# Kernel tuning notes

Hardware: AMD Instinct MI355X
Metric: run time of the kernel (lower is better)

The kernel has to match this reference:

```python
import jax, jax.numpy as jnp
import numpy as np
import math

HIDDEN = 1024
HEADS = 16
LAYERS = 4
IN_DIM = 512
OUT_DIM = 1024
B, S = 4, 2048


def _pos_encoding(seq_len, dim):
    pos = jnp.arange(seq_len, dtype=jnp.float32)[:, None]            # [S,1]
    div = jnp.exp(jnp.arange(0, dim, 2, dtype=jnp.float32) * (-math.log(10000.0) / dim))  # [D/2]
    ang = pos * div                                                   # [S,D/2]
    # interleave: even idx sin, odd idx cos
    return jnp.stack([jnp.sin(ang), jnp.cos(ang)], axis=-1).reshape(seq_len, dim)


def _layernorm(x, g, b, eps=1e-5):
    mu = jnp.mean(x, axis=-1, keepdims=True)
    var = jnp.var(x, axis=-1, keepdims=True)
    return (x - mu) * jax.lax.rsqrt(var + eps) * g + b


def setup_inputs() -> dict:
    key = jax.random.key(0)
    ks = jax.random.split(key, 8)
    d = {
        'x': jax.random.normal(ks[0], (B, S, IN_DIM), jnp.float32),
        'in_W': jax.random.normal(ks[1], (IN_DIM, HIDDEN), jnp.float32) * (1.0 / math.sqrt(IN_DIM)),
        'in_b': jnp.zeros((HIDDEN,), jnp.float32),
        'qkv_W': jax.random.normal(ks[2], (LAYERS, HIDDEN, 3 * HIDDEN), jnp.float32) * (1.0 / math.sqrt(HIDDEN)),
        'qkv_b': jnp.zeros((LAYERS, 3 * HIDDEN), jnp.float32),
        'out_W': jax.random.normal(ks[3], (LAYERS, HIDDEN, HIDDEN), jnp.float32) * (1.0 / math.sqrt(HIDDEN)),
        'out_b': jnp.zeros((LAYERS, HIDDEN), jnp.float32),
        'ln1_g': jnp.ones((LAYERS, HIDDEN), jnp.float32),
        'ln1_b': jnp.zeros((LAYERS, HIDDEN), jnp.float32),
        'ln2_g': jnp.ones((LAYERS, HIDDEN), jnp.float32),
        'ln2_b': jnp.zeros((LAYERS, HIDDEN), jnp.float32),
        'ff1_W': jax.random.normal(ks[4], (LAYERS, HIDDEN, 4 * HIDDEN), jnp.float32) * (1.0 / math.sqrt(HIDDEN)),
        'ff1_b': jnp.zeros((LAYERS, 4 * HIDDEN), jnp.float32),
        'ff2_W': jax.random.normal(ks[5], (LAYERS, 4 * HIDDEN, HIDDEN), jnp.float32) * (1.0 / math.sqrt(4 * HIDDEN)),
        'ff2_b': jnp.zeros((LAYERS, HIDDEN), jnp.float32),
        'fin_g': jnp.ones((HIDDEN,), jnp.float32),
        'fin_b': jnp.zeros((HIDDEN,), jnp.float32),
        'op_W': jax.random.normal(ks[6], (HIDDEN, OUT_DIM), jnp.float32) * (1.0 / math.sqrt(HIDDEN)),
        'op_b': jnp.zeros((OUT_DIM,), jnp.float32),
    }
    return d


def reference(x, in_W, in_b, qkv_W, qkv_b, out_W, out_b, ln1_g, ln1_b, ln2_g, ln2_b,
              ff1_W, ff1_b, ff2_W, ff2_b, fin_g, fin_b, op_W, op_b):
    b, s, _ = x.shape
    dh = HIDDEN // HEADS
    h = x @ in_W + in_b                                   # [B,S,D]
    h = h * math.sqrt(HIDDEN) + _pos_encoding(s, HIDDEN)  # scaled + PE (dropout=eval)
    for i in range(LAYERS):
        qkv = (h @ qkv_W[i] + qkv_b[i]).reshape(b, s, 3, HEADS, dh)
        q, k, v = qkv[:, :, 0], qkv[:, :, 1], qkv[:, :, 2]
        scores = jnp.einsum('bqhd,bkhd->bhqk', q, k) / math.sqrt(dh)
        attn = jax.nn.softmax(scores, axis=-1)
        ctx = jnp.einsum('bhqk,bkhd->bqhd', attn, v).reshape(b, s, HIDDEN)
        h = _layernorm(h + (ctx @ out_W[i] + out_b[i]), ln1_g[i], ln1_b[i])
        ff = jax.nn.relu(h @ ff1_W[i] + ff1_b[i]) @ ff2_W[i] + ff2_b[i]
        h = _layernorm(h + ff, ln2_g[i], ln2_b[i])
    h = _layernorm(h, fin_g, fin_b)
    return h @ op_W + op_b
```

## Files before the change

### kernel.cpp

```cpp
#include <hip/hip_runtime.h>
#include <math.h>

typedef unsigned short u16;
typedef __attribute__((ext_vector_type(8))) __bf16 bf16x8;
typedef __attribute__((ext_vector_type(4))) float floatx4;
typedef unsigned int __attribute__((address_space(1))) g_u32;
typedef unsigned int __attribute__((address_space(3))) l_u32;

#define EPI_BIAS  1
#define EPI_RELU  2
#define EPI_EMBED 8

__device__ __forceinline__ float bf2f(u16 u) {
    union { unsigned int i; float f; } v; v.i = ((unsigned int)u) << 16; return v.f;
}
__device__ __forceinline__ u16 f2bf(float f) {
    union { __bf16 b; u16 u; } v; v.b = (__bf16)f; return v.u;
}
__device__ __forceinline__ void gl_lds16(const void* g, void* l) {
    __builtin_amdgcn_global_load_lds((const g_u32*)g, (l_u32*)l, 16, 0, 0);
}
__device__ __forceinline__ float posenc(int s, int c) {
    double e = exp((double)(c & 1022) * (-9.210340371976184 / 1024.0));
    double ang = (double)s * e;
    return (float)((c & 1) ? cos(ang) : sin(ang));
}

__global__ __launch_bounds__(256) void conv_split(
    const float* __restrict__ in, u16* __restrict__ oh, u16* __restrict__ ol) {
    const int i = (blockIdx.x * 256 + threadIdx.x) * 8;
    float4 a = ((const float4*)(in + i))[0];
    float4 b = ((const float4*)(in + i))[1];
    float f[8] = {a.x, a.y, a.z, a.w, b.x, b.y, b.z, b.w};
    union { u16 u[8]; uint4 q; } H, L;
    #pragma unroll
    for (int j = 0; j < 8; ++j) {
        u16 hi = f2bf(f[j]);
        H.u[j] = hi; L.u[j] = f2bf(f[j] - bf2f(hi));
    }
    *(uint4*)&oh[i] = H.q;
    *(uint4*)&ol[i] = L.q;
}

template<int TMODE>
__global__ __launch_bounds__(256) void transpose_f2b(
    const float* __restrict__ in, u16* __restrict__ oh,
    int R, int C) {
    __shared__ float tile[32][33];
    int bx = blockIdx.x * 32, by = blockIdx.y * 32;
    int tx = threadIdx.x & 31, ty = threadIdx.x >> 5;
    #pragma unroll
    for (int i = ty; i < 32; i += 8) tile[i][tx] = in[(size_t)(by + i) * C + bx + tx];
    __syncthreads();
    #pragma unroll
    for (int i = ty; i < 32; i += 8) {
        float f = tile[tx][i];
        u16 hi = f2bf(f);
        u16 o = (TMODE == 2) ? f2bf(f - bf2f(hi)) : hi;
        oh[(size_t)(bx + i) * R + by + tx] = o;
    }
}

template<int EPI, bool ACCUM, bool WF, bool WB, bool WB2>
__global__ __launch_bounds__(256) void gemm_k(
    const u16* __restrict__ A, const u16* __restrict__ Bt,
    const float* __restrict__ bias,
    float* __restrict__ outF, u16* __restrict__ outB, u16* __restrict__ outB2,
    int M, int N, int K) {
    __shared__ alignas(16) u16 As[128 * 32];
    __shared__ alignas(16) u16 Bs[128 * 32];
    const int tid = threadIdx.x;
    const int wave = tid >> 6, lane = tid & 63;
    const int l16 = lane & 15, quad = lane >> 4;
    const int bm = blockIdx.x * 128, bn = blockIdx.y * 128;
    const int wm = (wave & 1) * 64, wn = (wave >> 1) * 64;
    const int sr = tid >> 2, sc = (tid & 3) * 8;

    floatx4 acc[4][4];
    floatx4 zero = {0.0f, 0.0f, 0.0f, 0.0f};
    #pragma unroll
    for (int i = 0; i < 4; ++i)
        #pragma unroll
        for (int j = 0; j < 4; ++j) acc[i][j] = zero;

    for (int k0 = 0; k0 < K; k0 += 32) {
        #pragma unroll
        for (int p = 0; p < 2; ++p) {
            const u16* ga = A + (size_t)(bm + sr + 64 * p) * K + k0 + sc;
            gl_lds16(ga, &As[(p * 64 + (wave << 4)) * 32]);
        }
        #pragma unroll
        for (int p = 0; p < 2; ++p) {
            const u16* gb = Bt + (size_t)(bn + sr + 64 * p) * K + k0 + sc;
            gl_lds16(gb, &Bs[(p * 64 + (wave << 4)) * 32]);
        }
        __syncthreads();
        bf16x8 af[4], bfr[4];
        #pragma unroll
        for (int i = 0; i < 4; ++i) af[i] = *(const bf16x8*)&As[(wm + i * 16 + l16) * 32 + quad * 8];
        #pragma unroll
        for (int j = 0; j < 4; ++j) bfr[j] = *(const bf16x8*)&Bs[(wn + j * 16 + l16) * 32 + quad * 8];
        #pragma unroll
        for (int i = 0; i < 4; ++i)
            #pragma unroll
            for (int j = 0; j < 4; ++j)
                acc[i][j] = __builtin_amdgcn_mfma_f32_16x16x32_bf16(af[i], bfr[j], acc[i][j], 0, 0, 0);
        __syncthreads();
    }

    #pragma unroll
    for (int i = 0; i < 4; ++i) {
        #pragma unroll
        for (int r = 0; r < 4; ++r) {
            int row = bm + wm + i * 16 + quad * 4 + r;
            #pragma unroll
            for (int j = 0; j < 4; ++j) {
                int col = bn + wn + j * 16 + l16;
                float v = acc[i][j][r];
                if (EPI & EPI_BIAS) v += bias[col];
                if (ACCUM) v += outF[(size_t)row * N + col];
                if (EPI & EPI_EMBED) { v = v * 32.0f + posenc(row & 2047, col); }
                if (EPI & EPI_RELU) v = fmaxf(v, 0.0f);
                if (WF) outF[(size_t)row * N + col] = v;
                if (WB) {
                    u16 hi = f2bf(v);
                    outB[(size_t)row * N + col] = hi;
                    if (WB2) outB2[(size_t)row * N + col] = f2bf(v - bf2f(hi));
                }
            }
        }
    }
}

template<bool SPLIT>
__global__ __launch_bounds__(256) void attn_k(
    const float* __restrict__ qkv, u16* __restrict__ ctx) {
    constexpr int KSTR = 72;
    constexpr int VSTR = 72;
    constexpr int PSTR = 88;
    __shared__ alignas(16) u16 Kh[2][64 * KSTR];
    __shared__ alignas(16) u16 Kl[2][SPLIT ? 64 * KSTR : 8];
    __shared__ alignas(16) u16 Vt[2][64 * VSTR];
    __shared__ alignas(16) u16 Ps[128 * PSTR];

    const int tid = threadIdx.x, wave = tid >> 6, lane = tid & 63;
    const int l16 = lane & 15, quad = lane >> 4;
    const int bh = blockIdx.x >> 4, qt = blockIdx.x & 15;
    const int b = bh >> 4, h = bh & 15;
    const size_t base = (size_t)b * 2048 * 3072;
    const int wq = wave * 32;

    const int kr = tid >> 2, kcb = (tid & 3) * 16;
    const float* gK = qkv + base + (size_t)kr * 3072 + 1024 + h * 64 + kcb;
    const int vk = lane, vdg = wave * 16;
    const float* gV = qkv + base + (size_t)vk * 3072 + 2048 + h * 64 + vdg;

    bf16x8 qh[2][2], ql[2][2];
    #pragma unroll
    for (int i = 0; i < 2; ++i) {
        const float* g = qkv + base + (size_t)(qt * 128 + wq + i * 16 + l16) * 3072 + h * 64 + quad * 8;
        #pragma unroll
        for (int kk = 0; kk < 2; ++kk) {
            float4 va = ((const float4*)(g + kk * 32))[0];
            float4 vb = ((const float4*)(g + kk * 32))[1];
            float f[8] = {va.x, va.y, va.z, va.w, vb.x, vb.y, vb.z, vb.w};
            union { u16 u[8]; bf16x8 v; } th, tl;
            #pragma unroll
            for (int j = 0; j < 8; ++j) {
                float s = f[j] * 0.125f;
                u16 hi = f2bf(s);
                th.u[j] = hi;
                if (SPLIT) tl.u[j] = f2bf(s - bf2f(hi));
            }
            qh[i][kk] = th.v;
            if (SPLIT) ql[i][kk] = tl.v;
        }
    }

    float4 pk4[4], pv4[4];
    auto LOAD = [&](int c) {
        const float* g = gK + (size_t)(c * 64) * 3072;
        pk4[0] = ((const float4*)g)[0]; pk4[1] = ((const float4*)g)[1];
        pk4[2] = ((const float4*)g)[2]; pk4[3] = ((const float4*)g)[3];
        const float* g2 = gV + (size_t)(c * 64) * 3072;
        pv4[0] = ((const float4*)g2)[0]; pv4[1] = ((const float4*)g2)[1];
        pv4[2] = ((const float4*)g2)[2]; pv4[3] = ((const float4*)g2)[3];
    };
    auto STORE = [&](int bu) {
        const float* pf = (const float*)pk4;
        union { u16 u[8]; uint4 q; } h0, h1, s0, s1;
        #pragma unroll
        for (int j = 0; j < 8; ++j) {
            float a = pf[j], c2 = pf[8 + j];
            u16 ah = f2bf(a); h0.u[j] = ah;
            u16 ch = f2bf(c2); h1.u[j] = ch;
            if (SPLIT) { s0.u[j] = f2bf(a - bf2f(ah)); s1.u[j] = f2bf(c2 - bf2f(ch)); }
        }
        *(uint4*)&Kh[bu][kr * KSTR + kcb]     = h0.q;
        *(uint4*)&Kh[bu][kr * KSTR + kcb + 8] = h1.q;
        if (SPLIT) {
            *(uint4*)&Kl[bu][kr * KSTR + kcb]     = s0.q;
            *(uint4*)&Kl[bu][kr * KSTR + kcb + 8] = s1.q;
        }
        const float* vf = (const float*)pv4;
        #pragma unroll
        for (int j = 0; j < 16; ++j)
            Vt[bu][(vdg + j) * VSTR + vk] = f2bf(vf[j]);
    };

    floatx4 acc_o[2][4];
    float mrun[2][4], lrun[2][4];
    floatx4 zf = {0.0f, 0.0f, 0.0f, 0.0f};
    #pragma unroll
    for (int i = 0; i < 2; ++i)
        #pragma unroll
        for (int j = 0; j < 4; ++j) acc_o[i][j] = zf;
    #pragma unroll
    for (int i = 0; i < 2; ++i)
        #pragma unroll
        for (int r = 0; r < 4; ++r) { mrun[i][r] = -1e30f; lrun[i][r] = 0.0f; }

    LOAD(0); STORE(0); LOAD(1);
    __syncthreads();

    for (int c = 0; c < 32; ++c) {
        const int cur = c & 1;

        floatx4 acc_s[2][4];
        #pragma unroll
        for (int i = 0; i < 2; ++i)
            #pragma unroll
            for (int j = 0; j < 4; ++j) acc_s[i][j] = zf;
        #pragma unroll
        for (int kk = 0; kk < 2; ++kk) {
            bf16x8 kbh[4], kbl[4];
            #pragma unroll
            for (int j = 0; j < 4; ++j) {
                kbh[j] = *(const bf16x8*)&Kh[cur][(j * 16 + l16) * KSTR + kk * 32 + quad * 8];
                if (SPLIT) kbl[j] = *(const bf16x8*)&Kl[cur][(j * 16 + l16) * KSTR + kk * 32 + quad * 8];
            }
            __builtin_amdgcn_s_setprio(1);
            #pragma unroll
            for (int i = 0; i < 2; ++i)
                #pragma unroll
                for (int j = 0; j < 4; ++j) {
                    acc_s[i][j] = __builtin_amdgcn_mfma_f32_16x16x32_bf16(qh[i][kk], kbh[j], acc_s[i][j], 0, 0, 0);
                    if (SPLIT) {
                        acc_s[i][j] = __builtin_amdgcn_mfma_f32_16x16x32_bf16(ql[i][kk], kbh[j], acc_s[i][j], 0, 0, 0);
                        acc_s[i][j] = __builtin_amdgcn_mfma_f32_16x16x32_bf16(qh[i][kk], kbl[j], acc_s[i][j], 0, 0, 0);
                    }
                }
            __builtin_amdgcn_s_setprio(0);
        }

        float mx[2][4];
        #pragma unroll
        for (int i = 0; i < 2; ++i)
            #pragma unroll
            for (int r = 0; r < 4; ++r) {
                float m0 = fmaxf(fmaxf(acc_s[i][0][r], acc_s[i][1][r]),
                                 fmaxf(acc_s[i][2][r], acc_s[i][3][r]));
                #pragma unroll
                for (int off = 8; off; off >>= 1) m0 = fmaxf(m0, __shfl_xor(m0, off));
                mx[i][r] = m0;
            }
        bool up = false;
        #pragma unroll
        for (int i = 0; i < 2; ++i)
            #pragma unroll
            for (int r = 0; r < 4; ++r) up = up || (mx[i][r] > mrun[i][r] + 8.0f);
        if (__any(up)) {
            #pragma unroll
            for (int i = 0; i < 2; ++i)
                #pragma unroll
                for (int r = 0; r < 4; ++r) {
                    float nm = fmaxf(mrun[i][r], mx[i][r]);
                    float sc = __expf(mrun[i][r] - nm);
                    mrun[i][r] = nm;
                    lrun[i][r] *= sc;
                    #pragma unroll
                    for (int jd = 0; jd < 4; ++jd) acc_o[i][jd][r] *= sc;
                }
        }
        #pragma unroll
        for (int i = 0; i < 2; ++i)
            #pragma unroll
            for (int r = 0; r < 4; ++r) {
                float rs = 0.0f;
                #pragma unroll
                for (int j = 0; j < 4; ++j) {
                    float p = __expf(acc_s[i][j][r] - mrun[i][r]);
                    acc_s[i][j][r] = p;
                    rs += p;
                }
                #pragma unroll
                for (int off = 8; off; off >>= 1) rs += __shfl_xor(rs, off);
                lrun[i][r] += rs;
                #pragma unroll
                for (int j = 0; j < 4; ++j)
                    Ps[(wq + i * 16 + quad * 4 + r) * PSTR + j * 16 + l16] = f2bf(acc_s[i][j][r]);
            }
        asm volatile("s_waitcnt lgkmcnt(0)" ::: "memory");

        #pragma unroll
        for (int kk = 0; kk < 2; ++kk) {
            bf16x8 pa[2], vb[4];
            #pragma unroll
            for (int i = 0; i < 2; ++i)
                pa[i] = *(const bf16x8*)&Ps[(wq + i * 16 + l16) * PSTR + kk * 32 + quad * 8];
            #pragma unroll
            for (int jd = 0; jd < 4; ++jd)
                vb[jd] = *(const bf16x8*)&Vt[cur][(jd * 16 + l16) * VSTR + kk * 32 + quad * 8];
            __builtin_amdgcn_s_setprio(1);
            #pragma unroll
            for (int i = 0; i < 2; ++i)
                #pragma unroll
                for (int jd = 0; jd < 4; ++jd)
                    acc_o[i][jd] = __builtin_amdgcn_mfma_f32_16x16x32_bf16(pa[i], vb[jd], acc_o[i][jd], 0, 0, 0);
            __builtin_amdgcn_s_setprio(0);
        }

        if (c + 1 < 32) STORE(cur ^ 1);
        __syncthreads();
        if (c + 2 < 32) LOAD(c + 2);
    }

    #pragma unroll
    for (int i = 0; i < 2; ++i) {
        #pragma unroll
        for (int r = 0; r < 4; ++r) {
            float inv = 1.0f / lrun[i][r];
            size_t ro = (size_t)(b * 2048 + qt * 128 + wq + i * 16 + quad * 4 + r) * 1024 + h * 64;
            #pragma unroll
            for (int jd = 0; jd < 4; ++jd)
                ctx[ro + jd * 16 + l16] = f2bf(acc_o[i][jd][r] * inv);
        }
    }
}

__global__ __launch_bounds__(256) void ln_k(
    float* __restrict__ h, const float* __restrict__ g, const float* __restrict__ bb,
    u16* __restrict__ hb) {
    const int row = blockIdx.x, tid = threadIdx.x;
    const int wave = tid >> 6, lane = tid & 63;
    float4 v = *(const float4*)(h + (size_t)row * 1024 + tid * 4);
    float x[4] = {v.x, v.y, v.z, v.w};
    float s = x[0] + x[1] + x[2] + x[3];
    float s2 = x[0] * x[0] + x[1] * x[1] + x[2] * x[2] + x[3] * x[3];
    for (int off = 32; off; off >>= 1) { s += __shfl_xor(s, off); s2 += __shfl_xor(s2, off); }
    __shared__ float red[8];
    if (lane == 0) { red[wave] = s; red[4 + wave] = s2; }
    __syncthreads();
    s = red[0] + red[1] + red[2] + red[3];
    s2 = red[4] + red[5] + red[6] + red[7];
    float mu = s * (1.0f / 1024.0f);
    float var = s2 * (1.0f / 1024.0f) - mu * mu;
    float rs = rsqrtf(var + 1e-5f);
    float4 gg = *(const float4*)(g + tid * 4);
    float4 bp = *(const float4*)(bb + tid * 4);
    float4 o;
    o.x = (x[0] - mu) * rs * gg.x + bp.x;
    o.y = (x[1] - mu) * rs * gg.y + bp.y;
    o.z = (x[2] - mu) * rs * gg.z + bp.z;
    o.w = (x[3] - mu) * rs * gg.w + bp.w;
    *(float4*)(h + (size_t)row * 1024 + tid * 4) = o;
    union { u16 u[4]; uint2 q; } hb4;
    hb4.u[0] = f2bf(o.x); hb4.u[1] = f2bf(o.y);
    hb4.u[2] = f2bf(o.z); hb4.u[3] = f2bf(o.w);
    *(uint2*)&hb[(size_t)row * 1024 + tid * 4] = hb4.q;
}

extern "C" void kernel_launch(void* const* d_in, const int* in_sizes, int n_in,
                              void* d_out, int out_size, void* d_ws, size_t ws_size,
                              hipStream_t stream) {
    const float* x     = (const float*)d_in[0];
    const float* in_W  = (const float*)d_in[1];
    const float* in_b  = (const float*)d_in[2];
    const float* qkv_W = (const float*)d_in[3];
    const float* qkv_b = (const float*)d_in[4];
    const float* out_W = (const float*)d_in[5];
    const float* out_b = (const float*)d_in[6];
    const float* ln1_g = (const float*)d_in[7];
    const float* ln1_b = (const float*)d_in[8];
    const float* ln2_g = (const float*)d_in[9];
    const float* ln2_b = (const float*)d_in[10];
    const float* ff1_W = (const float*)d_in[11];
    const float* ff1_b = (const float*)d_in[12];
    const float* ff2_W = (const float*)d_in[13];
    const float* ff2_b = (const float*)d_in[14];
    const float* fin_g = (const float*)d_in[15];
    const float* fin_b = (const float*)d_in[16];
    const float* op_W  = (const float*)d_in[17];
    const float* op_b  = (const float*)d_in[18];

    size_t off = 0;
    char* wsb = (char*)d_ws;
    auto alloc = [&](size_t bytes) { void* p = wsb + off; off += (bytes + 255) & ~(size_t)255; return p; };
    u16*   BtH  = (u16*)alloc((size_t)4096 * 1024 * 2);
    float* hbuf = (float*)alloc((size_t)8192 * 1024 * 4);
    float* qkvb = (float*)alloc((size_t)8192 * 3072 * 4);
    u16*   ctxb = (u16*)alloc((size_t)8192 * 1024 * 2);
    u16*   hbfH = (u16*)alloc((size_t)8192 * 1024 * 2);
    if (off > ws_size) return;
    u16* xh  = (u16*)qkvb;
    u16* xl  = xh + (size_t)8192 * 512;
    u16* h0h = ctxb;
    u16* h0l = hbfH;
    u16* ffb = (u16*)qkvb;

    dim3 tb(256);

    conv_split<<<dim3(2048), tb, 0, stream>>>(x, xh, xl);
    transpose_f2b<0><<<dim3(32, 16), tb, 0, stream>>>(in_W, BtH, 512, 1024);
    gemm_k<0, false, true, false, false><<<dim3(64, 8), tb, 0, stream>>>(
        xh, BtH, nullptr, hbuf, nullptr, nullptr, 8192, 1024, 512);
    gemm_k<0, true, true, false, false><<<dim3(64, 8), tb, 0, stream>>>(
        xl, BtH, nullptr, hbuf, nullptr, nullptr, 8192, 1024, 512);
    transpose_f2b<2><<<dim3(32, 16), tb, 0, stream>>>(in_W, BtH, 512, 1024);
    gemm_k<EPI_BIAS | EPI_EMBED, true, true, true, true><<<dim3(64, 8), tb, 0, stream>>>(
        xh, BtH, in_b, hbuf, h0h, h0l, 8192, 1024, 512);

    for (int L = 0; L < 4; ++L) {
        if (L == 0) {
            transpose_f2b<0><<<dim3(96, 32), tb, 0, stream>>>(qkv_W, BtH, 1024, 3072);
            gemm_k<0, false, true, false, false><<<dim3(64, 24), tb, 0, stream>>>(
                h0h, BtH, nullptr, qkvb, nullptr, nullptr, 8192, 3072, 1024);
            gemm_k<0, true, true, false, false><<<dim3(64, 24), tb, 0, stream>>>(
                h0l, BtH, nullptr, qkvb, nullptr, nullptr, 8192, 3072, 1024);
            transpose_f2b<2><<<dim3(96, 32), tb, 0, stream>>>(qkv_W, BtH, 1024, 3072);
            gemm_k<EPI_BIAS, true, true, false, false><<<dim3(64, 24), tb, 0, stream>>>(
                h0h, BtH, qkv_b, qkvb, nullptr, nullptr, 8192, 3072, 1024);
        } else {
            transpose_f2b<0><<<dim3(96, 32), tb, 0, stream>>>(
                qkv_W + (size_t)L * 1024 * 3072, BtH, 1024, 3072);
            gemm_k<EPI_BIAS, false, true, false, false><<<dim3(64, 24), tb, 0, stream>>>(
                hbfH, BtH, qkv_b + (size_t)L * 3072, qkvb, nullptr, nullptr, 8192, 3072, 1024);
        }
        if (L == 0) attn_k<true><<<dim3(1024), tb, 0, stream>>>(qkvb, ctxb);
        else        attn_k<false><<<dim3(1024), tb, 0, stream>>>(qkvb, ctxb);
        transpose_f2b<0><<<dim3(32, 32), tb, 0, stream>>>(
            out_W + (size_t)L * 1024 * 1024, BtH, 1024, 1024);
        gemm_k<EPI_BIAS, true, true, false, false><<<dim3(64, 8), tb, 0, stream>>>(
            ctxb, BtH, out_b + (size_t)L * 1024, hbuf, nullptr, nullptr, 8192, 1024, 1024);
        ln_k<<<8192, tb, 0, stream>>>(hbuf, ln1_g + (size_t)L * 1024, ln1_b + (size_t)L * 1024, hbfH);
        transpose_f2b<0><<<dim3(128, 32), tb, 0, stream>>>(
            ff1_W + (size_t)L * 1024 * 4096, BtH, 1024, 4096);
        gemm_k<EPI_BIAS | EPI_RELU, false, false, true, false><<<dim3(64, 32), tb, 0, stream>>>(
            hbfH, BtH, ff1_b + (size_t)L * 4096, nullptr, ffb, nullptr, 8192, 4096, 1024);
        transpose_f2b<0><<<dim3(32, 128), tb, 0, stream>>>(
            ff2_W + (size_t)L * 4096 * 1024, BtH, 4096, 1024);
        gemm_k<EPI_BIAS, true, true, false, false><<<dim3(64, 8), tb, 0, stream>>>(
            ffb, BtH, ff2_b + (size_t)L * 1024, hbuf, nullptr, nullptr, 8192, 1024, 4096);
        ln_k<<<8192, tb, 0, stream>>>(hbuf, ln2_g + (size_t)L * 1024, ln2_b + (size_t)L * 1024, hbfH);
    }

    ln_k<<<8192, tb, 0, stream>>>(hbuf, fin_g, fin_b, hbfH);
    transpose_f2b<0><<<dim3(32, 32), tb, 0, stream>>>(op_W, BtH, 1024, 1024);
    gemm_k<EPI_BIAS, false, true, false, false><<<dim3(64, 8), tb, 0, stream>>>(
        hbfH, BtH, op_b, (float*)d_out, nullptr, nullptr, 8192, 1024, 1024);
}
```

Baseline: 2.937 ms.

## Emit bf16 QKV for later layers and use async-LDS attention with pre-transposed V

For layers 1-3, the QKV GEMM now writes bf16 directly instead of fp32. A new kernel transposes V per head, and a new attention kernel stages K and V into swizzled LDS with global_load_lds and double buffering, replacing register-staged fp32 loads and on-the-fly conversion. The aim is to halve QKV write and read traffic and cut conversion and LDS-store work in attention. The cost is an extra transpose pass and some precision loss, since Q is rounded to bf16 before the scale. Layer 0 keeps the old split-precision kernel, now without the template.

```diff
diff --git a/kernel.cpp b/kernel.cpp
--- a/kernel.cpp
+++ b/kernel.cpp
@@ -59,6 +59,23 @@
         u16 o = (TMODE == 2) ? f2bf(f - bf2f(hi)) : hi;
         oh[(size_t)(bx + i) * R + by + tx] = o;
     }
+}
+
+__global__ __launch_bounds__(256) void transpose_v(
+    const u16* __restrict__ q16, u16* __restrict__ vT) {
+    __shared__ u16 tile[32][33];
+    const int bh = blockIdx.y;
+    const int b = bh >> 4, h = bh & 15;
+    const int s0 = (blockIdx.x & 63) * 32;
+    const int d0 = (blockIdx.x >> 6) * 32;
+    const int tx = threadIdx.x & 31, ty = threadIdx.x >> 5;
+    #pragma unroll
+    for (int i = ty; i < 32; i += 8)
+        tile[i][tx] = q16[(size_t)(b * 2048 + s0 + i) * 3072 + 2048 + h * 64 + d0 + tx];
+    __syncthreads();
+    #pragma unroll
+    for (int i = ty; i < 32; i += 8)
+        vT[((size_t)bh * 64 + d0 + i) * 2048 + s0 + tx] = tile[tx][i];
 }
 
 template<int EPI, bool ACCUM, bool WF, bool WB, bool WB2>
@@ -132,14 +149,13 @@
     }
 }
 
-template<bool SPLIT>
 __global__ __launch_bounds__(256) void attn_k(
     const float* __restrict__ qkv, u16* __restrict__ ctx) {
     constexpr int KSTR = 72;
     constexpr int VSTR = 72;
     constexpr int PSTR = 88;
     __shared__ alignas(16) u16 Kh[2][64 * KSTR];
-    __shared__ alignas(16) u16 Kl[2][SPLIT ? 64 * KSTR : 8];
+    __shared__ alignas(16) u16 Kl[2][64 * KSTR];
     __shared__ alignas(16) u16 Vt[2][64 * VSTR];
     __shared__ alignas(16) u16 Ps[128 * PSTR];
 
@@ -170,10 +186,9 @@
                 float s = f[j] * 0.125f;
                 u16 hi = f2bf(s);
                 th.u[j] = hi;
-                if (SPLIT) tl.u[j] = f2bf(s - bf2f(hi));
-            }
-            qh[i][kk] = th.v;
-            if (SPLIT) ql[i][kk] = tl.v;
+                tl.u[j] = f2bf(s - bf2f(hi));
+            }
+            qh[i][kk] = th.v; ql[i][kk] = tl.v;
         }
     }
 
@@ -192,16 +207,13 @@
         #pragma unroll
         for (int j = 0; j < 8; ++j) {
             float a = pf[j], c2 = pf[8 + j];
-            u16 ah = f2bf(a); h0.u[j] = ah;
-            u16 ch = f2bf(c2); h1.u[j] = ch;
-            if (SPLIT) { s0.u[j] = f2bf(a - bf2f(ah)); s1.u[j] = f2bf(c2 - bf2f(ch)); }
+            u16 ah = f2bf(a); h0.u[j] = ah; s0.u[j] = f2bf(a - bf2f(ah));
+            u16 ch = f2bf(c2); h1.u[j] = ch; s1.u[j] = f2bf(c2 - bf2f(ch));
         }
         *(uint4*)&Kh[bu][kr * KSTR + kcb]     = h0.q;
         *(uint4*)&Kh[bu][kr * KSTR + kcb + 8] = h1.q;
-        if (SPLIT) {
-            *(uint4*)&Kl[bu][kr * KSTR + kcb]     = s0.q;
-            *(uint4*)&Kl[bu][kr * KSTR + kcb + 8] = s1.q;
-        }
+        *(uint4*)&Kl[bu][kr * KSTR + kcb]     = s0.q;
+        *(uint4*)&Kl[bu][kr * KSTR + kcb + 8] = s1.q;
         const float* vf = (const float*)pv4;
         #pragma unroll
         for (int j = 0; j < 16; ++j)
@@ -237,7 +249,7 @@
             #pragma unroll
             for (int j = 0; j < 4; ++j) {
                 kbh[j] = *(const bf16x8*)&Kh[cur][(j * 16 + l16) * KSTR + kk * 32 + quad * 8];
-                if (SPLIT) kbl[j] = *(const bf16x8*)&Kl[cur][(j * 16 + l16) * KSTR + kk * 32 + quad * 8];
+                kbl[j] = *(const bf16x8*)&Kl[cur][(j * 16 + l16) * KSTR + kk * 32 + quad * 8];
             }
             __builtin_amdgcn_s_setprio(1);
             #pragma unroll
@@ -245,10 +257,8 @@
                 #pragma unroll
                 for (int j = 0; j < 4; ++j) {
                     acc_s[i][j] = __builtin_amdgcn_mfma_f32_16x16x32_bf16(qh[i][kk], kbh[j], acc_s[i][j], 0, 0, 0);
-                    if (SPLIT) {
-                        acc_s[i][j] = __builtin_amdgcn_mfma_f32_16x16x32_bf16(ql[i][kk], kbh[j], acc_s[i][j], 0, 0, 0);
-                        acc_s[i][j] = __builtin_amdgcn_mfma_f32_16x16x32_bf16(qh[i][kk], kbl[j], acc_s[i][j], 0, 0, 0);
-                    }
+                    acc_s[i][j] = __builtin_amdgcn_mfma_f32_16x16x32_bf16(ql[i][kk], kbh[j], acc_s[i][j], 0, 0, 0);
+                    acc_s[i][j] = __builtin_amdgcn_mfma_f32_16x16x32_bf16(qh[i][kk], kbl[j], acc_s[i][j], 0, 0, 0);
                 }
             __builtin_amdgcn_s_setprio(0);
         }
@@ -323,6 +333,176 @@
         if (c + 1 < 32) STORE(cur ^ 1);
         __syncthreads();
         if (c + 2 < 32) LOAD(c + 2);
+    }
+
+    #pragma unroll
+    for (int i = 0; i < 2; ++i) {
+        #pragma unroll
+        for (int r = 0; r < 4; ++r) {
+            float inv = 1.0f / lrun[i][r];
+            size_t ro = (size_t)(b * 2048 + qt * 128 + wq + i * 16 + quad * 4 + r) * 1024 + h * 64;
+            #pragma unroll
+            for (int jd = 0; jd < 4; ++jd)
+                ctx[ro + jd * 16 + l16] = f2bf(acc_o[i][jd][r] * inv);
+        }
+    }
+}
+
+__global__ __launch_bounds__(256) void attn2_k(
+    const u16* __restrict__ qkvh, const u16* __restrict__ vT,
+    u16* __restrict__ ctx) {
+    constexpr int PSTR = 72;
+    __shared__ alignas(16) u16 Kh[2][64 * 64];
+    __shared__ alignas(16) u16 Vt[2][64 * 64];
+    __shared__ alignas(16) u16 Ps[128 * PSTR];
+
+    const int tid = threadIdx.x, wave = tid >> 6, lane = tid & 63;
+    const int l16 = lane & 15, quad = lane >> 4;
+    const int bh = blockIdx.x >> 4, qt = blockIdx.x & 15;
+    const int b = bh >> 4, h = bh & 15;
+    const int wq = wave * 32;
+
+    const int r8 = tid >> 3;
+    const int cusw = (tid & 7) ^ (r8 & 7);
+    const u16* gK = qkvh + (size_t)(b * 2048 + r8) * 3072 + 1024 + h * 64 + cusw * 8;
+    const u16* gV = vT + ((size_t)bh * 64 + r8) * 2048 + cusw * 8;
+    const int ldst = (wave << 9);
+
+    auto STAGE = [&](int c, int bu) {
+        #pragma unroll
+        for (int p = 0; p < 2; ++p) {
+            gl_lds16(gK + (size_t)(c * 64 + p * 32) * 3072, &Kh[bu][p * 2048 + ldst]);
+            gl_lds16(gV + (size_t)(p * 32) * 2048 + c * 64, &Vt[bu][p * 2048 + ldst]);
+        }
+    };
+
+    bf16x8 qh[2][2];
+    #pragma unroll
+    for (int i = 0; i < 2; ++i) {
+        const u16* g = qkvh + (size_t)(b * 2048 + qt * 128 + wq + i * 16 + l16) * 3072 + h * 64;
+        #pragma unroll
+        for (int kk = 0; kk < 2; ++kk) {
+            union { u16 u[8]; bf16x8 v; uint4 q; } t;
+            t.q = *(const uint4*)(g + kk * 32 + quad * 8);
+            #pragma unroll
+            for (int j = 0; j < 8; ++j) t.u[j] = f2bf(bf2f(t.u[j]) * 0.125f);
+            qh[i][kk] = t.v;
+        }
+    }
+
+    floatx4 acc_o[2][4];
+    float mrun[2][4], lrun[2][4];
+    floatx4 zf = {0.0f, 0.0f, 0.0f, 0.0f};
+    #pragma unroll
+    for (int i = 0; i < 2; ++i)
+        #pragma unroll
+        for (int j = 0; j < 4; ++j) acc_o[i][j] = zf;
+    #pragma unroll
+    for (int i = 0; i < 2; ++i)
+        #pragma unroll
+        for (int r = 0; r < 4; ++r) { mrun[i][r] = -1e30f; lrun[i][r] = 0.0f; }
+
+    STAGE(0, 0);
+    __syncthreads();
+
+    for (int c = 0; c < 32; ++c) {
+        const int cur = c & 1;
+        if (c + 1 < 32) STAGE(c + 1, cur ^ 1);
+
+        floatx4 acc_s[2][4];
+        #pragma unroll
+        for (int i = 0; i < 2; ++i)
+            #pragma unroll
+            for (int j = 0; j < 4; ++j) acc_s[i][j] = zf;
+        #pragma unroll
+        for (int kk = 0; kk < 2; ++kk) {
+            bf16x8 kb[4];
+            #pragma unroll
+            for (int j = 0; j < 4; ++j) {
+                int row = j * 16 + l16;
+                int cu = (kk * 4 + quad) ^ (row & 7);
+                kb[j] = *(const bf16x8*)&Kh[cur][row * 64 + cu * 8];
+            }
+            __builtin_amdgcn_s_setprio(1);
+            #pragma unroll
+            for (int i = 0; i < 2; ++i)
+                #pragma unroll
+                for (int j = 0; j < 4; ++j)
+                    acc_s[i][j] = __builtin_amdgcn_mfma_f32_16x16x32_bf16(qh[i][kk], kb[j], acc_s[i][j], 0, 0, 0);
+            __builtin_amdgcn_s_setprio(0);
+        }
+
+        float mx[2][4];
+        #pragma unroll
+        for (int i = 0; i < 2; ++i)
+            #pragma unroll
+            for (int r = 0; r < 4; ++r) {
+                float m0 = fmaxf(fmaxf(acc_s[i][0][r], acc_s[i][1][r]),
+                                 fmaxf(acc_s[i][2][r], acc_s[i][3][r]));
+                #pragma unroll
+                for (int off = 8; off; off >>= 1) m0 = fmaxf(m0, __shfl_xor(m0, off));
+                mx[i][r] = m0;
+            }
+        bool up = false;
+        #pragma unroll
+        for (int i = 0; i < 2; ++i)
+            #pragma unroll
+            for (int r = 0; r < 4; ++r) up = up || (mx[i][r] > mrun[i][r] + 8.0f);
+        if (__any(up)) {
+            #pragma unroll
+            for (int i = 0; i < 2; ++i)
+                #pragma unroll
+                for (int r = 0; r < 4; ++r) {
+                    float nm = fmaxf(mrun[i][r], mx[i][r]);
+                    float sc = __expf(mrun[i][r] - nm);
+                    mrun[i][r] = nm;
+                    lrun[i][r] *= sc;
+                    #pragma unroll
+                    for (int jd = 0; jd < 4; ++jd) acc_o[i][jd][r] *= sc;
+                }
+        }
+        #pragma unroll
+        for (int i = 0; i < 2; ++i)
+            #pragma unroll
+            for (int r = 0; r < 4; ++r) {
+                float rs = 0.0f;
+                #pragma unroll
+                for (int j = 0; j < 4; ++j) {
+                    float p = __expf(acc_s[i][j][r] - mrun[i][r]);
+                    acc_s[i][j][r] = p;
+                    rs += p;
+                }
+                #pragma unroll
+                for (int off = 8; off; off >>= 1) rs += __shfl_xor(rs, off);
+                lrun[i][r] += rs;
+                #pragma unroll
+                for (int j = 0; j < 4; ++j)
+                    Ps[(wq + i * 16 + quad * 4 + r) * PSTR + j * 16 + l16] = f2bf(acc_s[i][j][r]);
+            }
+        asm volatile("s_waitcnt lgkmcnt(0)" ::: "memory");
+
+        #pragma unroll
+        for (int kk = 0; kk < 2; ++kk) {
+            bf16x8 pa[2], vb[4];
+            #pragma unroll
+            for (int i = 0; i < 2; ++i)
+                pa[i] = *(const bf16x8*)&Ps[(wq + i * 16 + l16) * PSTR + kk * 32 + quad * 8];
+            #pragma unroll
+            for (int jd = 0; jd < 4; ++jd) {
+                int row = jd * 16 + l16;
+                int cu = (kk * 4 + quad) ^ (row & 7);
+                vb[jd] = *(const bf16x8*)&Vt[cur][row * 64 + cu * 8];
+            }
+            __builtin_amdgcn_s_setprio(1);
+            #pragma unroll
+            for (int i = 0; i < 2; ++i)
+                #pragma unroll
+                for (int jd = 0; jd < 4; ++jd)
+                    acc_o[i][jd] = __builtin_amdgcn_mfma_f32_16x16x32_bf16(pa[i], vb[jd], acc_o[i][jd], 0, 0, 0);
+            __builtin_amdgcn_s_setprio(0);
+        }
+
+        __syncthreads();
     }
 
     #pragma unroll
@@ -402,11 +582,13 @@
     u16*   ctxb = (u16*)alloc((size_t)8192 * 1024 * 2);
     u16*   hbfH = (u16*)alloc((size_t)8192 * 1024 * 2);
     if (off > ws_size) return;
-    u16* xh  = (u16*)qkvb;
-    u16* xl  = xh + (size_t)8192 * 512;
-    u16* h0h = ctxb;
-    u16* h0l = hbfH;
-    u16* ffb = (u16*)qkvb;
+    u16* xh   = (u16*)qkvb;
+    u16* xl   = xh + (size_t)8192 * 512;
+    u16* h0h  = ctxb;
+    u16* h0l  = hbfH;
+    u16* qkvH = (u16*)qkvb;
+    u16* vTb  = hbfH;
+    u16* ffb  = (u16*)qkvb;
 
     dim3 tb(256);
 
@@ -430,14 +612,15 @@
             transpose_f2b<2><<<dim3(96, 32), tb, 0, stream>>>(qkv_W, BtH, 1024, 3072);
             gemm_k<EPI_BIAS, true, true, false, false><<<dim3(64, 24), tb, 0, stream>>>(
                 h0h, BtH, qkv_b, qkvb, nullptr, nullptr, 8192, 3072, 1024);
+            attn_k<<<dim3(1024), tb, 0, stream>>>(qkvb, ctxb);
         } else {
             transpose_f2b<0><<<dim3(96, 32), tb, 0, stream>>>(
                 qkv_W + (size_t)L * 1024 * 3072, BtH, 1024, 3072);
-            gemm_k<EPI_BIAS, false, true, false, false><<<dim3(64, 24), tb, 0, stream>>>(
-                hbfH, BtH, qkv_b + (size_t)L * 3072, qkvb, nullptr, nullptr, 8192, 3072, 1024);
-        }
-        if (L == 0) attn_k<true><<<dim3(1024), tb, 0, stream>>>(qkvb, ctxb);
-        else        attn_k<false><<<dim3(1024), tb, 0, stream>>>(qkvb, ctxb);
+            gemm_k<EPI_BIAS, false, false, true, false><<<dim3(64, 24), tb, 0, stream>>>(
+                hbfH, BtH, qkv_b + (size_t)L * 3072, nullptr, qkvH, nullptr, 8192, 3072, 1024);
+            transpose_v<<<dim3(128, 64), tb, 0, stream>>>(qkvH, vTb);
+            attn2_k<<<dim3(1024), tb, 0, stream>>>(qkvH, vTb, ctxb);
+        }
         transpose_f2b<0><<<dim3(32, 32), tb, 0, stream>>>(
             out_W + (size_t)L * 1024 * 1024, BtH, 1024, 1024);
         gemm_k<EPI_BIAS, true, true, false, false><<<dim3(64, 8), tb, 0, stream>>>(
```

New measurement: 2.936 ms. About the same (-0.0%).
